# Kernel optimization log

Hardware: AMD Instinct MI355X
Metric: run time of the kernel (lower is better)

The kernel has to match this reference:

```python
import jax, jax.numpy as jnp
import numpy as np

NUM_ITERATIONS = 10
ALPHA = 0.1


def setup_inputs() -> dict:
    key = jax.random.key(0)
    k1, k2, k3, k4 = jax.random.split(key, 4)
    N, E, F_IN, H = 100000, 3200000, 512, 64
    x = jax.random.normal(k1, (N, F_IN), dtype=jnp.float32)
    edge_index = jax.random.randint(k2, (2, E), 0, N, dtype=jnp.int32)
    edge_weight = jnp.ones((E,), dtype=jnp.float32)
    # glorot-ish scaled dense weights
    W0 = jax.random.normal(k3, (F_IN, H), dtype=jnp.float32) * (2.0 / (F_IN + H)) ** 0.5
    b0 = jnp.zeros((H,), dtype=jnp.float32)
    W1 = jax.random.normal(k4, (H, H), dtype=jnp.float32) * (2.0 / (H + H)) ** 0.5
    b1 = jnp.zeros((H,), dtype=jnp.float32)
    return {"x": x, "edge_index": edge_index, "edge_weight": edge_weight,
            "W0": W0, "b0": b0, "W1": W1, "b1": b1}


def _gcn_norm_edge(edge_index, edge_weight, num_nodes):
    # renorm: add self-loops with weight 1, then symmetric D^-1/2 A D^-1/2
    row, col = edge_index[0], edge_index[1]
    loop = jnp.arange(num_nodes, dtype=edge_index.dtype)
    row = jnp.concatenate([row, loop])
    col = jnp.concatenate([col, loop])
    w = jnp.concatenate([edge_weight, jnp.ones((num_nodes,), edge_weight.dtype)])
    deg = jax.ops.segment_sum(w, row, num_segments=num_nodes)
    dinv = jnp.where(deg > 0, jax.lax.rsqrt(jnp.where(deg > 0, deg, 1.0)), 0.0)
    w_norm = dinv[row] * w * dinv[col]
    return row, col, w_norm


def reference(x, edge_index, edge_weight, W0, b0, W1, b1):
    N = x.shape[0]
    # MLP: hidden layers relu-activated, last layer unactivated
    h = jax.nn.relu(x @ W0 + b0)
    h = h @ W1 + b1  # [N, H]

    row, col, w_norm = _gcn_norm_edge(edge_index, edge_weight, N)

    def step(z, _):
        # sparse propagation: gather at source, weight, scatter-add at dest
        msg = z[row] * w_norm[:, None]                      # [E+N, H]
        agg = jax.ops.segment_sum(msg, col, num_segments=N)  # [N, H]
        return (1.0 - ALPHA) * agg + ALPHA * h, None

    z, _ = jax.lax.scan(step, h, None, length=NUM_ITERATIONS)
    return z
```

## Files before the change

kernel.cpp:

```cpp
#include <hip/hip_runtime.h>


#define LDW 68
#define PAGE 16128
#define BPP 64

__device__ __forceinline__ float bf_lo(unsigned z) { return __uint_as_float(z << 16); }
__device__ __forceinline__ float bf_hi(unsigned z) { return __uint_as_float(z & 0xffff0000u); }
__device__ __forceinline__ unsigned bf_rne(float x) {
    unsigned u = __float_as_uint(x);
    return (u + 0x7fffu + ((u >> 16) & 1u)) >> 16;
}
__device__ __forceinline__ unsigned bf_pack(float x, float y) { return bf_rne(x) | (bf_rne(y) << 16); }

__global__ __launch_bounds__(256) void k_deg(const int* __restrict__ row, const float* __restrict__ ew,
                                             float* __restrict__ slab, int E, int chunk) {
    __shared__ float hf[PAGE];
    int p = blockIdx.x / BPP, b = blockIdx.x - p * BPP;
    int lo = p * PAGE;
    for (int i = threadIdx.x; i < PAGE; i += 256) hf[i] = 0.f;
    __syncthreads();
    int e0 = b * chunk, e1 = min(e0 + chunk, E);
    int evec = e0 + ((e1 - e0) & ~3);
    for (int e = e0 + (int)threadIdx.x * 4; e + 4 <= evec; e += 1024) {
        int4 r4 = *(const int4*)(row + e);
        float4 w4 = *(const float4*)(ew + e);
        unsigned a = (unsigned)(r4.x - lo), bq = (unsigned)(r4.y - lo);
        unsigned c = (unsigned)(r4.z - lo), dq = (unsigned)(r4.w - lo);
        if (a < PAGE) atomicAdd(&hf[a], w4.x);
        if (bq < PAGE) atomicAdd(&hf[bq], w4.y);
        if (c < PAGE) atomicAdd(&hf[c], w4.z);
        if (dq < PAGE) atomicAdd(&hf[dq], w4.w);
    }
    for (int e = evec + (int)threadIdx.x; e < e1; e += 256) {
        unsigned a = (unsigned)(row[e] - lo);
        if (a < PAGE) atomicAdd(&hf[a], ew[e]);
    }
    __syncthreads();
    float* out = slab + (size_t)blockIdx.x * PAGE;
    for (int i = threadIdx.x; i < PAGE; i += 256) out[i] = hf[i];
}

__global__ __launch_bounds__(256) void k_fold_deg(const float* __restrict__ slab, float* __restrict__ dinv, int N) {
    int i = blockIdx.x * 256 + threadIdx.x;
    if (i >= N) return;
    int p = i / PAGE, ld = i - p * PAGE;
    const float* base = slab + (size_t)(p * BPP) * PAGE + ld;
    float d = 1.0f;
#pragma unroll
    for (int b = 0; b < BPP; ++b) d += base[(size_t)b * PAGE];
    dinv[i] = d > 0.f ? rsqrtf(d) : 0.f;
}

__global__ __launch_bounds__(256) void k_cnt(const int* __restrict__ col, unsigned short* __restrict__ slab,
                                             int E, int chunk) {
    __shared__ int hi[PAGE];
    int p = blockIdx.x / BPP, b = blockIdx.x - p * BPP;
    int lo = p * PAGE;
    for (int i = threadIdx.x; i < PAGE; i += 256) hi[i] = 0;
    __syncthreads();
    int e0 = b * chunk, e1 = min(e0 + chunk, E);
    int evec = e0 + ((e1 - e0) & ~3);
    for (int e = e0 + (int)threadIdx.x * 4; e + 4 <= evec; e += 1024) {
        int4 c4 = *(const int4*)(col + e);
        unsigned a = (unsigned)(c4.x - lo), bq = (unsigned)(c4.y - lo);
        unsigned c = (unsigned)(c4.z - lo), dq = (unsigned)(c4.w - lo);
        if (a < PAGE) atomicAdd(&hi[a], 1);
        if (bq < PAGE) atomicAdd(&hi[bq], 1);
        if (c < PAGE) atomicAdd(&hi[c], 1);
        if (dq < PAGE) atomicAdd(&hi[dq], 1);
    }
    for (int e = evec + (int)threadIdx.x; e < e1; e += 256) {
        unsigned a = (unsigned)(col[e] - lo);
        if (a < PAGE) atomicAdd(&hi[a], 1);
    }
    __syncthreads();
    unsigned short* out = slab + (size_t)blockIdx.x * PAGE;
    for (int i = threadIdx.x; i < PAGE; i += 256) out[i] = (unsigned short)hi[i];
}

__global__ __launch_bounds__(256) void k_fold_cnt(unsigned short* __restrict__ slab, int* __restrict__ cnt, int N) {
    int i = blockIdx.x * 256 + threadIdx.x;
    if (i >= N) return;
    int p = i / PAGE, ld = i - p * PAGE;
    unsigned short* base = slab + (size_t)(p * BPP) * PAGE + ld;
    int run = 0;
#pragma unroll
    for (int b = 0; b < BPP; ++b) {
        size_t off = (size_t)b * PAGE;
        int v = base[off];
        base[off] = (unsigned short)run;
        run += v;
    }
    cnt[i] = run;
}

__global__ __launch_bounds__(256) void k_scanA(const int* __restrict__ cnt, int* __restrict__ csum, int N) {
    __shared__ int s[256];
    int t = threadIdx.x, base = blockIdx.x * 1024;
    int p = 0;
#pragma unroll
    for (int j = 0; j < 4; ++j) { int idx = base + t + 256 * j; if (idx < N) p += cnt[idx]; }
    s[t] = p; __syncthreads();
    for (int off = 128; off > 0; off >>= 1) { if (t < off) s[t] += s[t + off]; __syncthreads(); }
    if (t == 0) csum[blockIdx.x] = s[0];
}

__global__ __launch_bounds__(256) void k_scanB(int* __restrict__ csum, int NC) {
    __shared__ int s[256];
    int t = threadIdx.x;
    int v = (t < NC) ? csum[t] : 0;
    s[t] = v; __syncthreads();
    for (int off = 1; off < 256; off <<= 1) {
        int x = (t >= off) ? s[t - off] : 0;
        __syncthreads();
        s[t] += x; __syncthreads();
    }
    if (t < NC) csum[t] = s[t] - v;
}

__global__ __launch_bounds__(256) void k_scanC(const int* __restrict__ cnt, const int* __restrict__ csum,
                                               int* __restrict__ rowp, int N) {
    __shared__ int s[256];
    int t = threadIdx.x, base = blockIdx.x * 1024 + t * 4;
    int c0 = (base + 0 < N) ? cnt[base + 0] : 0;
    int c1 = (base + 1 < N) ? cnt[base + 1] : 0;
    int c2 = (base + 2 < N) ? cnt[base + 2] : 0;
    int c3 = (base + 3 < N) ? cnt[base + 3] : 0;
    int ts = c0 + c1 + c2 + c3;
    s[t] = ts; __syncthreads();
    for (int off = 1; off < 256; off <<= 1) {
        int x = (t >= off) ? s[t - off] : 0;
        __syncthreads();
        s[t] += x; __syncthreads();
    }
    int o = csum[blockIdx.x] + s[t] - ts;
    if (base + 0 < N) rowp[base + 0] = o;
    if (base + 1 < N) rowp[base + 1] = o + c0;
    if (base + 2 < N) rowp[base + 2] = o + c0 + c1;
    if (base + 3 < N) rowp[base + 3] = o + c0 + c1 + c2;
}

__global__ __launch_bounds__(256) void k_scat(const int* __restrict__ row, const int* __restrict__ col,
                                              const float* __restrict__ ew, const float* __restrict__ dinv,
                                              const int* __restrict__ rowp, const unsigned short* __restrict__ slab,
                                              unsigned* __restrict__ srcw, int E, int chunk) {
    __shared__ int cur[PAGE];
    int p = blockIdx.x / BPP, b = blockIdx.x - p * BPP;
    int lo = p * PAGE;
    for (int i = threadIdx.x; i < PAGE; i += 256) cur[i] = 0;
    __syncthreads();
    const unsigned short* soff = slab + (size_t)blockIdx.x * PAGE;
    int e0 = b * chunk, e1 = min(e0 + chunk, E);
    int evec = e0 + ((e1 - e0) & ~3);
    for (int e = e0 + (int)threadIdx.x * 4; e + 4 <= evec; e += 1024) {
        int4 c4 = *(const int4*)(col + e);
        unsigned a = (unsigned)(c4.x - lo), bq = (unsigned)(c4.y - lo);
        unsigned cc = (unsigned)(c4.z - lo), dq = (unsigned)(c4.w - lo);
        if ((a < PAGE) | (bq < PAGE) | (cc < PAGE) | (dq < PAGE)) {
            int4 r4 = *(const int4*)(row + e);
            float4 w4 = *(const float4*)(ew + e);
            if (a < PAGE) {
                int pos = rowp[c4.x] + soff[a] + atomicAdd(&cur[a], 1);
                srcw[pos] = ((unsigned)r4.x << 15) | (bf_rne(dinv[r4.x] * w4.x) & 0x7fffu);
            }
            if (bq < PAGE) {
                int pos = rowp[c4.y] + soff[bq] + atomicAdd(&cur[bq], 1);
                srcw[pos] = ((unsigned)r4.y << 15) | (bf_rne(dinv[r4.y] * w4.y) & 0x7fffu);
            }
            if (cc < PAGE) {
                int pos = rowp[c4.z] + soff[cc] + atomicAdd(&cur[cc], 1);
                srcw[pos] = ((unsigned)r4.z << 15) | (bf_rne(dinv[r4.z] * w4.z) & 0x7fffu);
            }
            if (dq < PAGE) {
                int pos = rowp[c4.w] + soff[dq] + atomicAdd(&cur[dq], 1);
                srcw[pos] = ((unsigned)r4.w << 15) | (bf_rne(dinv[r4.w] * w4.w) & 0x7fffu);
            }
        }
    }
    for (int e = evec + (int)threadIdx.x; e < e1; e += 256) {
        int c = col[e];
        unsigned a = (unsigned)(c - lo);
        if (a < PAGE) {
            int r = row[e];
            int pos = rowp[c] + soff[a] + atomicAdd(&cur[a], 1);
            srcw[pos] = ((unsigned)r << 15) | (bf_rne(dinv[r] * ew[e]) & 0x7fffu);
        }
    }
}

__global__ __launch_bounds__(256) void k_mlp(const float* __restrict__ x,
                                             const float* __restrict__ W0, const float* __restrict__ b0,
                                             const float* __restrict__ W1, const float* __restrict__ b1,
                                             unsigned* __restrict__ hb, int N) {
    __shared__ __align__(16) float xs[64 * LDW];
    __shared__ __align__(16) float ws[64 * LDW];
    int tid = threadIdx.x;
    int tc = tid & 15, tr = tid >> 4;
    int rbase = blockIdx.x * 64;

    float acc[4][4];
#pragma unroll
    for (int i = 0; i < 4; ++i)
#pragma unroll
        for (int j = 0; j < 4; ++j) acc[i][j] = 0.f;

    for (int ck = 0; ck < 8; ++ck) {
        int k0 = ck * 64;
#pragma unroll
        for (int j = 0; j < 4; ++j) {
            int l = tid + 256 * j;
            int r = l >> 4, kq = l & 15;
            int gr = rbase + r;
            float4 v = make_float4(0.f, 0.f, 0.f, 0.f);
            if (gr < N) v = *(const float4*)(x + (size_t)gr * 512 + k0 + kq * 4);
            xs[(kq * 4 + 0) * LDW + r] = v.x;
            xs[(kq * 4 + 1) * LDW + r] = v.y;
            xs[(kq * 4 + 2) * LDW + r] = v.z;
            xs[(kq * 4 + 3) * LDW + r] = v.w;
        }
#pragma unroll
        for (int j = 0; j < 4; ++j) {
            int l = tid + 256 * j;
            int kk = l >> 4, cq = l & 15;
            *(float4*)(ws + kk * LDW + cq * 4) = *(const float4*)(W0 + (size_t)(k0 + kk) * 64 + cq * 4);
        }
        __syncthreads();
#pragma unroll 4
        for (int k = 0; k < 64; ++k) {
            float4 a = *(const float4*)(xs + k * LDW + tr * 4);
            float4 w = *(const float4*)(ws + k * LDW + tc * 4);
            acc[0][0] = fmaf(a.x, w.x, acc[0][0]); acc[0][1] = fmaf(a.x, w.y, acc[0][1]);
            acc[0][2] = fmaf(a.x, w.z, acc[0][2]); acc[0][3] = fmaf(a.x, w.w, acc[0][3]);
            acc[1][0] = fmaf(a.y, w.x, acc[1][0]); acc[1][1] = fmaf(a.y, w.y, acc[1][1]);
            acc[1][2] = fmaf(a.y, w.z, acc[1][2]); acc[1][3] = fmaf(a.y, w.w, acc[1][3]);
            acc[2][0] = fmaf(a.z, w.x, acc[2][0]); acc[2][1] = fmaf(a.z, w.y, acc[2][1]);
            acc[2][2] = fmaf(a.z, w.z, acc[2][2]); acc[2][3] = fmaf(a.z, w.w, acc[2][3]);
            acc[3][0] = fmaf(a.w, w.x, acc[3][0]); acc[3][1] = fmaf(a.w, w.y, acc[3][1]);
            acc[3][2] = fmaf(a.w, w.z, acc[3][2]); acc[3][3] = fmaf(a.w, w.w, acc[3][3]);
        }
        __syncthreads();
    }
#pragma unroll
    for (int jj = 0; jj < 4; ++jj) {
        float b = b0[tc * 4 + jj];
        float4 v;
        v.x = fmaxf(acc[0][jj] + b, 0.f);
        v.y = fmaxf(acc[1][jj] + b, 0.f);
        v.z = fmaxf(acc[2][jj] + b, 0.f);
        v.w = fmaxf(acc[3][jj] + b, 0.f);
        *(float4*)(xs + (tc * 4 + jj) * LDW + tr * 4) = v;
    }
#pragma unroll
    for (int j = 0; j < 4; ++j) {
        int l = tid + 256 * j;
        int kk = l >> 4, cq = l & 15;
        *(float4*)(ws + kk * LDW + cq * 4) = *(const float4*)(W1 + (size_t)kk * 64 + cq * 4);
    }
    float acc2[4][4];
#pragma unroll
    for (int i = 0; i < 4; ++i)
#pragma unroll
        for (int j = 0; j < 4; ++j) acc2[i][j] = 0.f;
    __syncthreads();
#pragma unroll 4
    for (int k = 0; k < 64; ++k) {
        float4 a = *(const float4*)(xs + k * LDW + tr * 4);
        float4 w = *(const float4*)(ws + k * LDW + tc * 4);
        acc2[0][0] = fmaf(a.x, w.x, acc2[0][0]); acc2[0][1] = fmaf(a.x, w.y, acc2[0][1]);
        acc2[0][2] = fmaf(a.x, w.z, acc2[0][2]); acc2[0][3] = fmaf(a.x, w.w, acc2[0][3]);
        acc2[1][0] = fmaf(a.y, w.x, acc2[1][0]); acc2[1][1] = fmaf(a.y, w.y, acc2[1][1]);
        acc2[1][2] = fmaf(a.y, w.z, acc2[1][2]); acc2[1][3] = fmaf(a.y, w.w, acc2[1][3]);
        acc2[2][0] = fmaf(a.z, w.x, acc2[2][0]); acc2[2][1] = fmaf(a.z, w.y, acc2[2][1]);
        acc2[2][2] = fmaf(a.z, w.z, acc2[2][2]); acc2[2][3] = fmaf(a.z, w.w, acc2[2][3]);
        acc2[3][0] = fmaf(a.w, w.x, acc2[3][0]); acc2[3][1] = fmaf(a.w, w.y, acc2[3][1]);
        acc2[3][2] = fmaf(a.w, w.z, acc2[3][2]); acc2[3][3] = fmaf(a.w, w.w, acc2[3][3]);
    }
    float bv0 = b1[tc * 4 + 0], bv1 = b1[tc * 4 + 1], bv2 = b1[tc * 4 + 2], bv3 = b1[tc * 4 + 3];
#pragma unroll
    for (int i = 0; i < 4; ++i) {
        int gr = rbase + tr * 4 + i;
        if (gr < N) {
            float o0 = acc2[i][0] + bv0, o1 = acc2[i][1] + bv1;
            float o2 = acc2[i][2] + bv2, o3 = acc2[i][3] + bv3;
            *(uint2*)(hb + (size_t)gr * 32 + tc * 2) = make_uint2(bf_pack(o0, o1), bf_pack(o2, o3));
        }
    }
}

__global__ __launch_bounds__(256) void k_prop(const unsigned* __restrict__ srcw,
                                              const int* __restrict__ rowp, const int* __restrict__ cnt,
                                              const float* __restrict__ dinv,
                                              const unsigned* __restrict__ zin, const unsigned* __restrict__ hb,
                                              unsigned* __restrict__ zout_b, float* __restrict__ zout_f, int N) {
    int wid = (blockIdx.x << 2) | (threadIdx.x >> 6);
    int d = __builtin_amdgcn_readfirstlane(wid);
    if (d >= N) return;
    int lane = threadIdx.x & 63;
    int half = lane >> 5, fi = lane & 31;
    int beg = rowp[d], end = beg + cnt[d];
    float ax = 0.f, ay = 0.f;
    for (int e = beg + half; e < end; e += 16) {
        unsigned pk[8];
#pragma unroll
        for (int k = 0; k < 8; ++k) {
            int idx = e + 2 * k;
            pk[k] = srcw[min(idx, end - 1)];
        }
        unsigned z[8];
#pragma unroll
        for (int k = 0; k < 8; ++k) z[k] = zin[(pk[k] >> 15) * 32u + fi];
#pragma unroll
        for (int k = 0; k < 8; ++k) {
            float w = (e + 2 * k < end) ? __uint_as_float((pk[k] & 0x7fffu) << 16) : 0.f;
            ax = fmaf(w, bf_lo(z[k]), ax);
            ay = fmaf(w, bf_hi(z[k]), ay);
        }
    }
    ax += __shfl_xor(ax, 32);
    ay += __shfl_xor(ay, 32);
    if (half == 0) {
        float di = dinv[d];
        unsigned zs = zin[(size_t)d * 32 + fi];
        float s2 = di * di;
        float ox = 0.9f * fmaf(di, ax, s2 * bf_lo(zs));
        float oy = 0.9f * fmaf(di, ay, s2 * bf_hi(zs));
        unsigned hz = hb[(size_t)d * 32 + fi];
        ox = fmaf(0.1f, bf_lo(hz), ox);
        oy = fmaf(0.1f, bf_hi(hz), oy);
        if (zout_f) ((float2*)zout_f)[(size_t)d * 32 + fi] = make_float2(ox, oy);
        else zout_b[(size_t)d * 32 + fi] = bf_pack(ox, oy);
    }
}

extern "C" void kernel_launch(void* const* d_in, const int* in_sizes, int n_in,
                              void* d_out, int out_size, void* d_ws, size_t ws_size,
                              hipStream_t stream) {
    const float* x  = (const float*)d_in[0];
    const int*   ei = (const int*)d_in[1];
    const float* ew = (const float*)d_in[2];
    const float* W0 = (const float*)d_in[3];
    const float* b0 = (const float*)d_in[4];
    const float* W1 = (const float*)d_in[5];
    const float* b1 = (const float*)d_in[6];
    int N = in_sizes[0] / 512;
    int E = in_sizes[2];
    const int* row = ei;
    const int* col = ei + E;

    char* p = (char*)d_ws;
    auto alloc = [&](size_t bytes) -> char* {
        char* r = p;
        p += (bytes + 255) & ~(size_t)255;
        return r;
    };
    int NPg = (N + PAGE - 1) / PAGE;
    size_t zbytes = (size_t)N * 32 * 4;
    size_t slab_bytes = (size_t)NPg * BPP * PAGE * 4;
    unsigned* hb  = (unsigned*)alloc(zbytes);
    float* slabf  = (float*)alloc(slab_bytes);
    unsigned* srcw = (unsigned*)alloc((size_t)E * 4);
    float* dinv  = (float*)alloc((size_t)N * 4);
    int* cnt     = (int*)alloc((size_t)N * 4);
    int* rowp    = (int*)alloc((size_t)N * 4);
    int* csum    = (int*)alloc(512 * 4);
    unsigned short* slabu = (unsigned short*)slabf;
    unsigned* zb0 = (unsigned*)slabf;
    unsigned* zb1 = (unsigned*)((char*)slabf + zbytes);

    int gN = (N + 255) / 256;
    int NC = (N + 1023) / 1024;
    int chunk = (((E + BPP - 1) / BPP) + 3) & ~3;
    int gridPg = NPg * BPP;

    k_deg<<<gridPg, 256, 0, stream>>>(row, ew, slabf, E, chunk);
    k_fold_deg<<<gN, 256, 0, stream>>>(slabf, dinv, N);
    k_cnt<<<gridPg, 256, 0, stream>>>(col, slabu, E, chunk);
    k_fold_cnt<<<gN, 256, 0, stream>>>(slabu, cnt, N);
    k_scanA<<<NC, 256, 0, stream>>>(cnt, csum, N);
    k_scanB<<<1, 256, 0, stream>>>(csum, NC);
    k_scanC<<<NC, 256, 0, stream>>>(cnt, csum, rowp, N);
    k_scat<<<gridPg, 256, 0, stream>>>(row, col, ew, dinv, rowp, slabu, srcw, E, chunk);
    k_mlp<<<(N + 63) / 64, 256, 0, stream>>>(x, W0, b0, W1, b1, hb, N);

    unsigned* zbufs[2] = { zb0, zb1 };
    const unsigned* zi = hb;
    int gP = (N + 3) / 4;
    for (int it = 0; it < 10; ++it) {
        if (it < 9) {
            unsigned* zo = zbufs[it & 1];
            k_prop<<<gP, 256, 0, stream>>>(srcw, rowp, cnt, dinv, zi, hb, zo, nullptr, N);
            zi = zo;
        } else {
            k_prop<<<gP, 256, 0, stream>>>(srcw, rowp, cnt, dinv, zi, hb, nullptr, (float*)d_out, N);
        }
    }
}
```

Before: 1.170 ms.

## Use bf16 split-precision MFMA for the MLP with pre-transposed weights

Rewrites the two-layer MLP kernel to use bf16 16x16x32 MFMA instructions with a hi/lo bf16 split (three MFMAs per tile) to keep near-fp32 accuracy. A new conversion kernel transposes W0 and W1 into hi/lo bf16 buffers. The x tile is converted in registers and shared-memory FMA tiling is replaced, removing the scalar FMA cost of the 100k x 512 x 64 GEMM. It adds two small launches and bf16-split rounding error, and it reads x directly from global memory without shared staging. The first layer's output goes through shared memory as hi/lo halves.

```diff
diff --git a/kernel.cpp b/kernel.cpp
--- a/kernel.cpp
+++ b/kernel.cpp
@@ -1,9 +1,11 @@
 #include <hip/hip_runtime.h>
 
 
-#define LDW 68
 #define PAGE 16128
 #define BPP 64
+
+typedef __attribute__((ext_vector_type(8))) short bf16x8;
+typedef __attribute__((ext_vector_type(4))) float f32x4;
 
 __device__ __forceinline__ float bf_lo(unsigned z) { return __uint_as_float(z << 16); }
 __device__ __forceinline__ float bf_hi(unsigned z) { return __uint_as_float(z & 0xffff0000u); }
@@ -189,101 +191,115 @@
     }
 }
 
+__global__ __launch_bounds__(256) void k_wcvt(const float* __restrict__ W,
+                                              unsigned short* __restrict__ Th, unsigned short* __restrict__ Tl,
+                                              int K, int total) {
+    int i = blockIdx.x * 256 + threadIdx.x;
+    if (i >= total) return;
+    int k = i >> 6, n = i & 63;
+    float v = W[i];
+    unsigned hi = bf_rne(v);
+    float hv = __uint_as_float(hi << 16);
+    unsigned lo = bf_rne(v - hv);
+    Th[(size_t)n * K + k] = (unsigned short)hi;
+    Tl[(size_t)n * K + k] = (unsigned short)lo;
+}
+
 __global__ __launch_bounds__(256) void k_mlp(const float* __restrict__ x,
-                                             const float* __restrict__ W0, const float* __restrict__ b0,
-                                             const float* __restrict__ W1, const float* __restrict__ b1,
+                                             const unsigned short* __restrict__ w0th, const unsigned short* __restrict__ w0tl,
+                                             const unsigned short* __restrict__ w1th, const unsigned short* __restrict__ w1tl,
+                                             const float* __restrict__ b0, const float* __restrict__ b1,
                                              unsigned* __restrict__ hb, int N) {
-    __shared__ __align__(16) float xs[64 * LDW];
-    __shared__ __align__(16) float ws[64 * LDW];
+    __shared__ __align__(16) unsigned short h1h[64 * 72];
+    __shared__ __align__(16) unsigned short h1l[64 * 72];
     int tid = threadIdx.x;
-    int tc = tid & 15, tr = tid >> 4;
+    int w = tid >> 6, lane = tid & 63;
+    int g = lane >> 4, r16 = lane & 15;
     int rbase = blockIdx.x * 64;
-
-    float acc[4][4];
-#pragma unroll
-    for (int i = 0; i < 4; ++i)
-#pragma unroll
-        for (int j = 0; j < 4; ++j) acc[i][j] = 0.f;
-
-    for (int ck = 0; ck < 8; ++ck) {
-        int k0 = ck * 64;
-#pragma unroll
-        for (int j = 0; j < 4; ++j) {
-            int l = tid + 256 * j;
-            int r = l >> 4, kq = l & 15;
-            int gr = rbase + r;
-            float4 v = make_float4(0.f, 0.f, 0.f, 0.f);
-            if (gr < N) v = *(const float4*)(x + (size_t)gr * 512 + k0 + kq * 4);
-            xs[(kq * 4 + 0) * LDW + r] = v.x;
-            xs[(kq * 4 + 1) * LDW + r] = v.y;
-            xs[(kq * 4 + 2) * LDW + r] = v.z;
-            xs[(kq * 4 + 3) * LDW + r] = v.w;
-        }
-#pragma unroll
-        for (int j = 0; j < 4; ++j) {
-            int l = tid + 256 * j;
-            int kk = l >> 4, cq = l & 15;
-            *(float4*)(ws + kk * LDW + cq * 4) = *(const float4*)(W0 + (size_t)(k0 + kk) * 64 + cq * 4);
-        }
-        __syncthreads();
-#pragma unroll 4
-        for (int k = 0; k < 64; ++k) {
-            float4 a = *(const float4*)(xs + k * LDW + tr * 4);
-            float4 w = *(const float4*)(ws + k * LDW + tc * 4);
-            acc[0][0] = fmaf(a.x, w.x, acc[0][0]); acc[0][1] = fmaf(a.x, w.y, acc[0][1]);
-            acc[0][2] = fmaf(a.x, w.z, acc[0][2]); acc[0][3] = fmaf(a.x, w.w, acc[0][3]);
-            acc[1][0] = fmaf(a.y, w.x, acc[1][0]); acc[1][1] = fmaf(a.y, w.y, acc[1][1]);
-            acc[1][2] = fmaf(a.y, w.z, acc[1][2]); acc[1][3] = fmaf(a.y, w.w, acc[1][3]);
-            acc[2][0] = fmaf(a.z, w.x, acc[2][0]); acc[2][1] = fmaf(a.z, w.y, acc[2][1]);
-            acc[2][2] = fmaf(a.z, w.z, acc[2][2]); acc[2][3] = fmaf(a.z, w.w, acc[2][3]);
-            acc[3][0] = fmaf(a.w, w.x, acc[3][0]); acc[3][1] = fmaf(a.w, w.y, acc[3][1]);
-            acc[3][2] = fmaf(a.w, w.z, acc[3][2]); acc[3][3] = fmaf(a.w, w.w, acc[3][3]);
-        }
-        __syncthreads();
-    }
-#pragma unroll
-    for (int jj = 0; jj < 4; ++jj) {
-        float b = b0[tc * 4 + jj];
-        float4 v;
-        v.x = fmaxf(acc[0][jj] + b, 0.f);
-        v.y = fmaxf(acc[1][jj] + b, 0.f);
-        v.z = fmaxf(acc[2][jj] + b, 0.f);
-        v.w = fmaxf(acc[3][jj] + b, 0.f);
-        *(float4*)(xs + (tc * 4 + jj) * LDW + tr * 4) = v;
-    }
-#pragma unroll
-    for (int j = 0; j < 4; ++j) {
-        int l = tid + 256 * j;
-        int kk = l >> 4, cq = l & 15;
-        *(float4*)(ws + kk * LDW + cq * 4) = *(const float4*)(W1 + (size_t)kk * 64 + cq * 4);
-    }
-    float acc2[4][4];
-#pragma unroll
-    for (int i = 0; i < 4; ++i)
-#pragma unroll
-        for (int j = 0; j < 4; ++j) acc2[i][j] = 0.f;
-    __syncthreads();
-#pragma unroll 4
-    for (int k = 0; k < 64; ++k) {
-        float4 a = *(const float4*)(xs + k * LDW + tr * 4);
-        float4 w = *(const float4*)(ws + k * LDW + tc * 4);
-        acc2[0][0] = fmaf(a.x, w.x, acc2[0][0]); acc2[0][1] = fmaf(a.x, w.y, acc2[0][1]);
-        acc2[0][2] = fmaf(a.x, w.z, acc2[0][2]); acc2[0][3] = fmaf(a.x, w.w, acc2[0][3]);
-        acc2[1][0] = fmaf(a.y, w.x, acc2[1][0]); acc2[1][1] = fmaf(a.y, w.y, acc2[1][1]);
-        acc2[1][2] = fmaf(a.y, w.z, acc2[1][2]); acc2[1][3] = fmaf(a.y, w.w, acc2[1][3]);
-        acc2[2][0] = fmaf(a.z, w.x, acc2[2][0]); acc2[2][1] = fmaf(a.z, w.y, acc2[2][1]);
-        acc2[2][2] = fmaf(a.z, w.z, acc2[2][2]); acc2[2][3] = fmaf(a.z, w.w, acc2[2][3]);
-        acc2[3][0] = fmaf(a.w, w.x, acc2[3][0]); acc2[3][1] = fmaf(a.w, w.y, acc2[3][1]);
-        acc2[3][2] = fmaf(a.w, w.z, acc2[3][2]); acc2[3][3] = fmaf(a.w, w.w, acc2[3][3]);
-    }
-    float bv0 = b1[tc * 4 + 0], bv1 = b1[tc * 4 + 1], bv2 = b1[tc * 4 + 2], bv3 = b1[tc * 4 + 3];
-#pragma unroll
-    for (int i = 0; i < 4; ++i) {
-        int gr = rbase + tr * 4 + i;
-        if (gr < N) {
-            float o0 = acc2[i][0] + bv0, o1 = acc2[i][1] + bv1;
-            float o2 = acc2[i][2] + bv2, o3 = acc2[i][3] + bv3;
-            *(uint2*)(hb + (size_t)gr * 32 + tc * 2) = make_uint2(bf_pack(o0, o1), bf_pack(o2, o3));
+    int arow = rbase + w * 16 + r16;
+    bool rowok = arow < N;
+    const float* xp = x + (size_t)arow * 512 + g * 8;
+
+    f32x4 acc[4];
+#pragma unroll
+    for (int t = 0; t < 4; ++t) acc[t] = (f32x4){0.f, 0.f, 0.f, 0.f};
+
+    for (int ks = 0; ks < 16; ++ks) {
+        int k0 = ks * 32;
+        float4 v0 = make_float4(0.f, 0.f, 0.f, 0.f), v1 = v0;
+        if (rowok) {
+            v0 = *(const float4*)(xp + k0);
+            v1 = *(const float4*)(xp + k0 + 4);
+        }
+        float xv[8] = {v0.x, v0.y, v0.z, v0.w, v1.x, v1.y, v1.z, v1.w};
+        bf16x8 xh, xl;
+#pragma unroll
+        for (int e = 0; e < 8; ++e) {
+            float xe = xv[e];
+            unsigned hi = bf_rne(xe);
+            float hv = __uint_as_float(hi << 16);
+            unsigned lo = bf_rne(xe - hv);
+            xh[e] = (short)hi;
+            xl[e] = (short)lo;
+        }
+#pragma unroll
+        for (int t = 0; t < 4; ++t) {
+            size_t wo = (size_t)(t * 16 + r16) * 512 + k0 + g * 8;
+            bf16x8 wh = *(const bf16x8*)(w0th + wo);
+            bf16x8 wl = *(const bf16x8*)(w0tl + wo);
+            acc[t] = __builtin_amdgcn_mfma_f32_16x16x32_bf16(xh, wh, acc[t], 0, 0, 0);
+            acc[t] = __builtin_amdgcn_mfma_f32_16x16x32_bf16(xl, wh, acc[t], 0, 0, 0);
+            acc[t] = __builtin_amdgcn_mfma_f32_16x16x32_bf16(xh, wl, acc[t], 0, 0, 0);
+        }
+    }
+#pragma unroll
+    for (int t = 0; t < 4; ++t) {
+        int c = t * 16 + r16;
+        float bb = b0[c];
+#pragma unroll
+        for (int r = 0; r < 4; ++r) {
+            float v = fmaxf(acc[t][r] + bb, 0.f);
+            unsigned hi = bf_rne(v);
+            float hv = __uint_as_float(hi << 16);
+            unsigned lo = bf_rne(v - hv);
+            int rr = w * 16 + g * 4 + r;
+            h1h[rr * 72 + c] = (unsigned short)hi;
+            h1l[rr * 72 + c] = (unsigned short)lo;
+        }
+    }
+    __syncthreads();
+    f32x4 acc2[4];
+#pragma unroll
+    for (int t = 0; t < 4; ++t) acc2[t] = (f32x4){0.f, 0.f, 0.f, 0.f};
+#pragma unroll
+    for (int ks = 0; ks < 2; ++ks) {
+        int k0 = ks * 32;
+        const unsigned short* ap = h1h + (w * 16 + r16) * 72 + k0 + g * 8;
+        bf16x8 ah = *(const bf16x8*)ap;
+        bf16x8 al = *(const bf16x8*)(ap + 64 * 72);
+        al = *(const bf16x8*)(h1l + (w * 16 + r16) * 72 + k0 + g * 8);
+#pragma unroll
+        for (int t = 0; t < 4; ++t) {
+            size_t wo = (size_t)(t * 16 + r16) * 64 + k0 + g * 8;
+            bf16x8 wh = *(const bf16x8*)(w1th + wo);
+            bf16x8 wl = *(const bf16x8*)(w1tl + wo);
+            acc2[t] = __builtin_amdgcn_mfma_f32_16x16x32_bf16(ah, wh, acc2[t], 0, 0, 0);
+            acc2[t] = __builtin_amdgcn_mfma_f32_16x16x32_bf16(al, wh, acc2[t], 0, 0, 0);
+            acc2[t] = __builtin_amdgcn_mfma_f32_16x16x32_bf16(ah, wl, acc2[t], 0, 0, 0);
+        }
+    }
+    unsigned short* hb16 = (unsigned short*)hb;
+#pragma unroll
+    for (int t = 0; t < 4; ++t) {
+        int c = t * 16 + r16;
+        float bb = b1[c];
+#pragma unroll
+        for (int r = 0; r < 4; ++r) {
+            int grow = rbase + w * 16 + g * 4 + r;
+            if (grow < N) {
+                float v = acc2[t][r] + bb;
+                hb16[(size_t)grow * 64 + c] = (unsigned short)bf_rne(v);
+            }
         }
     }
 }
@@ -364,6 +380,10 @@
     int* cnt     = (int*)alloc((size_t)N * 4);
     int* rowp    = (int*)alloc((size_t)N * 4);
     int* csum    = (int*)alloc(512 * 4);
+    unsigned short* w0th = (unsigned short*)alloc(64 * 512 * 2);
+    unsigned short* w0tl = (unsigned short*)alloc(64 * 512 * 2);
+    unsigned short* w1th = (unsigned short*)alloc(64 * 64 * 2);
+    unsigned short* w1tl = (unsigned short*)alloc(64 * 64 * 2);
     unsigned short* slabu = (unsigned short*)slabf;
     unsigned* zb0 = (unsigned*)slabf;
     unsigned* zb1 = (unsigned*)((char*)slabf + zbytes);
@@ -373,6 +393,8 @@
     int chunk = (((E + BPP - 1) / BPP) + 3) & ~3;
     int gridPg = NPg * BPP;
 
+    k_wcvt<<<(512 * 64 + 255) / 256, 256, 0, stream>>>(W0, w0th, w0tl, 512, 512 * 64);
+    k_wcvt<<<(64 * 64 + 255) / 256, 256, 0, stream>>>(W1, w1th, w1tl, 64, 64 * 64);
     k_deg<<<gridPg, 256, 0, stream>>>(row, ew, slabf, E, chunk);
     k_fold_deg<<<gN, 256, 0, stream>>>(slabf, dinv, N);
     k_cnt<<<gridPg, 256, 0, stream>>>(col, slabu, E, chunk);
@@ -381,7 +403,7 @@
     k_scanB<<<1, 256, 0, stream>>>(csum, NC);
     k_scanC<<<NC, 256, 0, stream>>>(cnt, csum, rowp, N);
     k_scat<<<gridPg, 256, 0, stream>>>(row, col, ew, dinv, rowp, slabu, srcw, E, chunk);
-    k_mlp<<<(N + 63) / 64, 256, 0, stream>>>(x, W0, b0, W1, b1, hb, N);
+    k_mlp<<<(N + 63) / 64, 256, 0, stream>>>(x, w0th, w0tl, w1th, w1tl, b0, b1, hb, N);
 
     unsigned* zbufs[2] = { zb0, zb1 };
     const unsigned* zi = hb;
```

After: 1.216 ms. 4.0% more time.
